# Optimization experiments

Measured on AMD Instinct MI355X. Metric: run time of the kernel, lower is better.

Reference implementation:

```python
import jax, jax.numpy as jnp
import numpy as np

B, C, T, W, H = 32, 80, 2048, 128, 512
FRAMES_PER_WORD = T // W  # 16
K = 5  # conv kernel size (Component approximated as Conv1d(k=5)+ReLU)


def conv1d(x, w, b):
    # x: [B, Cin, T], w: [Cout, Cin, K] -> [B, Cout, T] (SAME padding)
    y = jax.lax.conv_general_dilated(
        x, w, window_strides=(1,), padding='SAME',
        dimension_numbers=('NCH', 'OIH', 'NCH'))
    return y + b[None, :, None]


def setup_inputs() -> dict:
    key = jax.random.key(0)
    k1, k2, k3 = jax.random.split(key, 3)
    features = jax.random.normal(k1, (B, C, T), dtype=jnp.float32)
    # word bounds: contiguous equal-length spans [start, end) covering all T frames
    starts = (jnp.arange(W, dtype=jnp.int64) * FRAMES_PER_WORD)
    ends = starts + FRAMES_PER_WORD
    word_bounds = jnp.broadcast_to(jnp.stack([starts, ends])[None], (B, 2, W))
    word_lengths = jnp.full((B,), W, dtype=jnp.int64)
    enc_w = jax.random.normal(k2, (H, C, K), dtype=jnp.float32) * 0.02
    enc_b = jnp.zeros((H,), dtype=jnp.float32)
    dec_w = jax.random.normal(k3, (1, H, K), dtype=jnp.float32) * 0.02
    dec_b = jnp.zeros((1,), dtype=jnp.float32)
    return {'features': features, 'word_bounds': word_bounds,
            'word_lengths': word_lengths, 'enc_w': enc_w, 'enc_b': enc_b,
            'dec_w': dec_w, 'dec_b': dec_b}


def reference(features, word_bounds, word_lengths, enc_w, enc_b, dec_w, dec_b):
    # Frame encoder: Conv1d + ReLU -> [B, H, T]
    frame_embedding = jax.nn.relu(conv1d(features, enc_w, enc_b))
    t = jnp.arange(T)
    start = word_bounds[:, 0, :]  # [B, W]
    end = word_bounds[:, 1, :]    # [B, W]
    # Ragged per-word mean pooling, fused as a masked matmul (segment mean).
    mask = (t[None, None, :] >= start[..., None]) & (t[None, None, :] < end[..., None])  # [B, W, T]
    valid = jnp.arange(W)[None, :] < word_lengths[:, None]  # [B, W]
    maskf = (mask & valid[..., None]).astype(frame_embedding.dtype)
    counts = jnp.maximum(maskf.sum(-1), 1.0)  # [B, W]
    word_embeddings = jnp.einsum('bct,bwt->bcw', frame_embedding, maskf) / counts[:, None, :]
    # Word decoder: Conv1d over the word axis -> [B, 1, W]
    return conv1d(word_embeddings, dec_w, dec_b)
```

## Files before the change

### kernel.cpp

```cpp
#include <hip/hip_runtime.h>

#define B_ 32
#define C_ 80
#define T_ 2048
#define W_ 128
#define H_ 512
#define K_ 5

#define KTOT 400
#define NKI  13
#define TM   128
#define TN   128
#define SF_STRIDE 80
#define SF_ROWS   136
#define SF_ELEMS  (SF_ROWS * SF_STRIDE)
#define ITER_STRIDE (2 * 4 * 64 * 8)
#define BF_ELEMS  (4 * NKI * ITER_STRIDE)

#define RB_FEAT   1024
#define RB_BFRAG  (RB_FEAT + BF_ELEMS / 256)
#define RB_WORDS  (RB_BFRAG + B_)

#define TILE_S 88

typedef _Float16 half8 __attribute__((ext_vector_type(8)));
typedef float    f4v   __attribute__((ext_vector_type(4)));

typedef const __attribute__((address_space(1))) unsigned int guint;
typedef __attribute__((address_space(3))) unsigned int luint;

__global__ __launch_bounds__(256) void prep_all(
    const float* __restrict__ feat, const float* __restrict__ enc_w,
    const int* __restrict__ bounds, const int* __restrict__ lengths,
    _Float16* __restrict__ featT, _Float16* __restrict__ Bf,
    int* __restrict__ word_of, float* __restrict__ inv_cnt)
{
    __shared__ _Float16 tile[64 * TILE_S];
    const int bid = blockIdx.x;
    const int tid = threadIdx.x;

    if (bid < RB_FEAT) {
        const int b = bid >> 5, tc = bid & 31;
        const int t0 = tc * 64;
        for (int idx = tid; idx < 80 * 64; idx += 256) {
            int cc = idx >> 6, tt = idx & 63;
            float v = feat[((size_t)b * C_ + cc) * T_ + t0 + tt];
            tile[tt * TILE_S + cc] = (_Float16)v;
        }
        __syncthreads();
        for (int idx = tid; idx < 64 * 10; idx += 256) {
            int tt = idx / 10, g = idx % 10;
            *(f4v*)(featT + ((size_t)b * T_ + t0 + tt) * C_ + g * 8) =
                *(const f4v*)(tile + tt * TILE_S + g * 8);
        }
    } else if (bid < RB_BFRAG) {
        int idx = (bid - RB_FEAT) * 256 + tid;
        int e  = idx & 7;
        int l  = (idx >> 3) & 63;
        int j  = (idx >> 9) & 3;
        int w2 = (idx >> 11) & 1;
        int it = (idx >> 12) % NKI;
        int nt = idx / (NKI << 12);
        int h  = nt * 128 + w2 * 64 + j * 16 + (l & 15);
        int kc = it * 32 + (l >> 4) * 8 + e;
        float v = 0.f;
        if (kc < KTOT) v = enc_w[(h * C_ + kc % 80) * K_ + kc / 80];
        Bf[idx] = (_Float16)v;
    } else {
        const int b = bid - RB_BFRAG;
        int* wob = word_of + b * T_;
        for (int t = tid; t < T_; t += 256) wob[t] = -1;
        __syncthreads();
        if (tid < W_) {
            const int len = lengths[b];
            int s = bounds[(b * 2 + 0) * W_ + tid];
            int e = bounds[(b * 2 + 1) * W_ + tid];
            s = max(s, 0); e = min(e, T_);
            bool valid = (tid < len) && (e > s);
            inv_cnt[b * W_ + tid] = valid ? 1.f / (float)(e - s) : 0.f;
            if (valid)
                for (int t = s; t < e; ++t) wob[t] = tid;
        }
    }
}

__global__ __launch_bounds__(256, 3) void gemm_enc(
    const _Float16* __restrict__ featT,
    const _Float16* __restrict__ Bf,
    const float*    __restrict__ enc_b,
    const int*      __restrict__ word_of,
    const float*    __restrict__ inv_cnt,
    float*          __restrict__ wemb)
{
    __shared__ __attribute__((aligned(16))) _Float16 sf[SF_ELEMS];

    const int tid = threadIdx.x;
    const int bid = blockIdx.x;
    const int xcd = bid & 7;
    const int u   = bid >> 3;
    const int nt  = u & 3;
    const int g   = xcd + ((u >> 2) << 3);
    const int b   = g >> 4;
    const int mt  = g & 15;
    const int t0 = mt * TM;
    const int h0 = nt * TN;

    const int lane = tid & 63;
    const int wid  = tid >> 6;
    const int wm = (wid >> 1) * 64;
    const int wn = (wid & 1) * 64;
    const int w2 = wid & 1;
    const int ml = lane & 15;
    const int q  = lane >> 4;

    {
        const _Float16* fb = featT + (size_t)b * T_ * C_;
        const int fbase = (t0 - 2) * C_;
        const int gmax  = T_ * C_ - 8;
        for (int ch = wid; ch < 22; ch += 4) {
            int loff = (ch << 9) + lane * 8;
            if (loff < SF_ELEMS) {
                int goff = fbase + loff;
                goff = min(max(goff, 0), gmax);
                __builtin_amdgcn_global_load_lds((guint*)(fb + goff),
                                                 (luint*)(sf + (ch << 9)), 16, 0, 0);
            }
        }
    }

    const int bT = b * T_;
    const int bW = b * W_;
    int wlo[4], whi[4];
    unsigned ownm = 0;
    {
        int wpv[4], wnx[4];
        #pragma unroll
        for (int i = 0; i < 4; ++i) {
            const int tg = t0 + wm + i * 16;
            wlo[i] = word_of[bT + tg];
            whi[i] = word_of[bT + tg + 15];
            wpv[i] = (tg == 0)       ? -2 : word_of[bT + tg - 1];
            wnx[i] = (tg + 16 >= T_) ? -2 : word_of[bT + tg + 16];
        }
        #pragma unroll
        for (int i = 0; i < 4; ++i)
            if (wpv[i] != wlo[i] && wnx[i] != wlo[i]) ownm |= (1u << i);
    }

    const half8* bfp = (const half8*)(Bf + (((nt * NKI) * 2 + w2) * 4 * 64 + lane) * 8);
    half8 bcur[4], bnxt[4];
    #pragma unroll
    for (int j = 0; j < 4; ++j) bcur[j] = bfp[j * 64];
    #pragma unroll
    for (int j = 0; j < 4; ++j) bnxt[j] = bfp[512 + j * 64];

    __syncthreads();

    if (mt == 0) {
        if (tid < 20) ((f4v*)sf)[tid] = (f4v){};
        __syncthreads();
    }
    if (mt == 15) {
        if (tid < 60) ((f4v*)(sf + 130 * SF_STRIDE))[tid] = (f4v){};
        __syncthreads();
    }

    f4v acc[4][4] = {};

    const int abase = (wm + ml) * SF_STRIDE + q * 8;

    half8 acur[4];
    #pragma unroll
    for (int i = 0; i < 4; ++i)
        acur[i] = *(const half8*)(sf + abase + i * 16 * SF_STRIDE);

    #pragma unroll
    for (int it = 0; it < NKI; ++it) {
        half8 anxt[4], bnn[4];
        #pragma unroll
        for (int i = 0; i < 4; ++i)
            anxt[i] = *(const half8*)(sf + abase + (it + 1) * 32 + i * 16 * SF_STRIDE);
        {
            const half8* bn = bfp + (it + 2) * 512;
            #pragma unroll
            for (int j = 0; j < 4; ++j) bnn[j] = bn[j * 64];
        }
        #pragma unroll
        for (int i = 0; i < 4; ++i)
            #pragma unroll
            for (int j = 0; j < 4; ++j)
                acc[i][j] = __builtin_amdgcn_mfma_f32_16x16x32_f16(acur[i], bcur[j], acc[i][j], 0, 0, 0);
        #pragma unroll
        for (int i = 0; i < 4; ++i) acur[i] = anxt[i];
        #pragma unroll
        for (int j = 0; j < 4; ++j) { bcur[j] = bnxt[j]; bnxt[j] = bnn[j]; }
    }

    float bias[4], invp[4];
    #pragma unroll
    for (int j = 0; j < 4; ++j) bias[j] = enc_b[h0 + wn + j * 16 + ml];
    #pragma unroll
    for (int i = 0; i < 4; ++i) invp[i] = inv_cnt[bW + max(wlo[i], 0)];

    #pragma unroll
    for (int i = 0; i < 4; ++i) {
        const int tg = t0 + wm + i * 16;
        const int w0  = wlo[i];
        const int w15 = whi[i];
        if (w0 == w15) {
            if (w0 >= 0) {
                const float inv = invp[i];
                const bool own = (ownm >> i) & 1;
                #pragma unroll
                for (int j = 0; j < 4; ++j) {
                    float s = 0.f;
                    #pragma unroll
                    for (int r = 0; r < 4; ++r) s += fmaxf(acc[i][j][r] + bias[j], 0.f);
                    s += __shfl_down(s, 32, 64);
                    s += __shfl_down(s, 16, 64);
                    if (q == 0) {
                        float val = s * inv;
                        float* dst = &wemb[(size_t)(bW + w0) * H_ + h0 + wn + j * 16 + ml];
                        if (own) *dst = val;
                        else atomicAdd(dst, val);
                    }
                }
            }
        } else {
            #pragma unroll
            for (int j = 0; j < 4; ++j) {
                #pragma unroll
                for (int r = 0; r < 4; ++r) {
                    int t = tg + q * 4 + r;
                    int w = word_of[bT + t];
                    if (w >= 0)
                        atomicAdd(&wemb[(size_t)(bW + w) * H_ + h0 + wn + j * 16 + ml],
                                  fmaxf(acc[i][j][r] + bias[j], 0.f) * inv_cnt[bW + w]);
                }
            }
        }
    }
}

__global__ __launch_bounds__(256) void dec_all(const float* __restrict__ wemb,
                                               const float* __restrict__ dec_w,
                                               const float* __restrict__ dec_b,
                                               float* __restrict__ out) {
    __shared__ float sdw[H_ * K_];
    __shared__ float se[16][8];
    const int bid = blockIdx.x;
    const int b = bid >> 4, ch = bid & 15;
    const int w0 = ch * 8;
    for (int idx = threadIdx.x; idx < H_ * K_; idx += 256) sdw[idx] = dec_w[idx];
    __syncthreads();
    const int wid = threadIdx.x >> 6, lane = threadIdx.x & 63;
    for (int row = wid; row < 12; row += 4) {
        int wq = w0 - 2 + row;
        float a[K_] = {};
        if (wq >= 0 && wq < W_) {
            const float* src = wemb + ((size_t)b * W_ + wq) * H_;
            #pragma unroll
            for (int r = 0; r < H_ / 64; ++r) {
                int h = r * 64 + lane;
                float v = src[h];
                #pragma unroll
                for (int k = 0; k < K_; ++k) a[k] += v * sdw[h * K_ + k];
            }
        }
        #pragma unroll
        for (int k = 0; k < K_; ++k) {
            #pragma unroll
            for (int off = 32; off > 0; off >>= 1) a[k] += __shfl_down(a[k], off, 64);
        }
        if (lane == 0) {
            #pragma unroll
            for (int k = 0; k < K_; ++k) se[row][k] = a[k];
        }
    }
    __syncthreads();
    if (threadIdx.x < 8) {
        int wl = threadIdx.x;
        float acc = dec_b[0];
        #pragma unroll
        for (int k = 0; k < K_; ++k) acc += se[wl + k][k];
        out[b * W_ + w0 + wl] = acc;
    }
}

extern "C" void kernel_launch(void* const* d_in, const int* in_sizes, int n_in,
                              void* d_out, int out_size, void* d_ws, size_t ws_size,
                              hipStream_t stream) {
    const float* feat    = (const float*)d_in[0];
    const int*   bounds  = (const int*)  d_in[1];
    const int*   lengths = (const int*)  d_in[2];
    const float* enc_w   = (const float*)d_in[3];
    const float* enc_b   = (const float*)d_in[4];
    const float* dec_w   = (const float*)d_in[5];
    const float* dec_b   = (const float*)d_in[6];
    float* out = (float*)d_out;

    char* p = (char*)d_ws;
    _Float16* featT = (_Float16*)p;  p += (size_t)B_ * T_ * C_ * 2;
    _Float16* Bf    = (_Float16*)p;  p += (size_t)(BF_ELEMS + 2 * ITER_STRIDE) * 2;
    int* word_of    = (int*)p;       p += (size_t)B_ * T_ * 4;
    float* inv_cnt  = (float*)p;     p += (size_t)B_ * W_ * 4;
    float* wemb     = (float*)p;

    prep_all<<<RB_WORDS, 256, 0, stream>>>(feat, enc_w, bounds, lengths,
                                           featT, Bf, word_of, inv_cnt);
    gemm_enc<<<B_ * (T_ / TM) * (H_ / TN), 256, 0, stream>>>(
        featT, Bf, enc_b, word_of, inv_cnt, wemb);
    dec_all<<<B_ * 16, 256, 0, stream>>>(wemb, dec_w, dec_b, out);
}
```

Measured before the change: 117.9 us.

## Loop over all H tiles per block to reuse staged feature tile

Each block now handles one (batch, time-tile) pair and loops over all four H tiles internally, reusing the shared-memory feature tile and word metadata instead of reloading them in four separate blocks. The grid shrinks to 512 blocks, and the occupancy hint is lowered to two blocks per CU to leave room for the extra bias registers. The block-to-XCD mapping is changed so each XCD handles four batches. The cost is fewer blocks to fill the GPU and a longer serial loop per block, which may reduce parallelism and latency hiding.

```diff
diff --git a/kernel.cpp b/kernel.cpp
--- a/kernel.cpp
+++ b/kernel.cpp
@@ -84,7 +84,7 @@
     }
 }
 
-__global__ __launch_bounds__(256, 3) void gemm_enc(
+__global__ __launch_bounds__(256, 2) void gemm_enc(
     const _Float16* __restrict__ featT,
     const _Float16* __restrict__ Bf,
     const float*    __restrict__ enc_b,
@@ -98,12 +98,9 @@
     const int bid = blockIdx.x;
     const int xcd = bid & 7;
     const int u   = bid >> 3;
-    const int nt  = u & 3;
-    const int g   = xcd + ((u >> 2) << 3);
-    const int b   = g >> 4;
-    const int mt  = g & 15;
+    const int b   = xcd * 4 + (u & 3);
+    const int mt  = u >> 2;
     const int t0 = mt * TM;
-    const int h0 = nt * TN;
 
     const int lane = tid & 63;
     const int wid  = tid >> 6;
@@ -146,13 +143,23 @@
         for (int i = 0; i < 4; ++i)
             if (wpv[i] != wlo[i] && wnx[i] != wlo[i]) ownm |= (1u << i);
     }
-
-    const half8* bfp = (const half8*)(Bf + (((nt * NKI) * 2 + w2) * 4 * 64 + lane) * 8);
+    float invp[4];
+    #pragma unroll
+    for (int i = 0; i < 4; ++i) invp[i] = inv_cnt[bW + max(wlo[i], 0)];
+
+    float biasAll[4][4];
+    #pragma unroll
+    for (int n = 0; n < 4; ++n)
+        #pragma unroll
+        for (int j = 0; j < 4; ++j)
+            biasAll[n][j] = enc_b[n * TN + wn + j * 16 + ml];
+
+    const half8* bfpB = (const half8*)(Bf + ((w2 * 4) * 64 + lane) * 8);
     half8 bcur[4], bnxt[4];
     #pragma unroll
-    for (int j = 0; j < 4; ++j) bcur[j] = bfp[j * 64];
+    for (int j = 0; j < 4; ++j) bcur[j] = bfpB[j * 64];
     #pragma unroll
-    for (int j = 0; j < 4; ++j) bnxt[j] = bfp[512 + j * 64];
+    for (int j = 0; j < 4; ++j) bnxt[j] = bfpB[512 + j * 64];
 
     __syncthreads();
 
@@ -165,77 +172,74 @@
         __syncthreads();
     }
 
-    f4v acc[4][4] = {};
-
     const int abase = (wm + ml) * SF_STRIDE + q * 8;
 
-    half8 acur[4];
-    #pragma unroll
-    for (int i = 0; i < 4; ++i)
-        acur[i] = *(const half8*)(sf + abase + i * 16 * SF_STRIDE);
-
-    #pragma unroll
-    for (int it = 0; it < NKI; ++it) {
-        half8 anxt[4], bnn[4];
+    for (int nt4 = 0; nt4 < 4; ++nt4) {
+        f4v acc[4][4] = {};
+
+        half8 acur[4];
         #pragma unroll
         for (int i = 0; i < 4; ++i)
-            anxt[i] = *(const half8*)(sf + abase + (it + 1) * 32 + i * 16 * SF_STRIDE);
-        {
-            const half8* bn = bfp + (it + 2) * 512;
-            #pragma unroll
-            for (int j = 0; j < 4; ++j) bnn[j] = bn[j * 64];
-        }
-        #pragma unroll
-        for (int i = 0; i < 4; ++i)
-            #pragma unroll
-            for (int j = 0; j < 4; ++j)
-                acc[i][j] = __builtin_amdgcn_mfma_f32_16x16x32_f16(acur[i], bcur[j], acc[i][j], 0, 0, 0);
-        #pragma unroll
-        for (int i = 0; i < 4; ++i) acur[i] = anxt[i];
-        #pragma unroll
-        for (int j = 0; j < 4; ++j) { bcur[j] = bnxt[j]; bnxt[j] = bnn[j]; }
-    }
-
-    float bias[4], invp[4];
-    #pragma unroll
-    for (int j = 0; j < 4; ++j) bias[j] = enc_b[h0 + wn + j * 16 + ml];
-    #pragma unroll
-    for (int i = 0; i < 4; ++i) invp[i] = inv_cnt[bW + max(wlo[i], 0)];
-
-    #pragma unroll
-    for (int i = 0; i < 4; ++i) {
-        const int tg = t0 + wm + i * 16;
-        const int w0  = wlo[i];
-        const int w15 = whi[i];
-        if (w0 == w15) {
-            if (w0 >= 0) {
-                const float inv = invp[i];
-                const bool own = (ownm >> i) & 1;
+            acur[i] = *(const half8*)(sf + abase + i * 16 * SF_STRIDE);
+
+        #pragma unroll
+        for (int it = 0; it < NKI; ++it) {
+            half8 anxt[4], bnn[4];
+            #pragma unroll
+            for (int i = 0; i < 4; ++i)
+                anxt[i] = *(const half8*)(sf + abase + (it + 1) * 32 + i * 16 * SF_STRIDE);
+            {
+                const half8* bn = bfpB + (nt4 * NKI + it + 2) * 512;
+                #pragma unroll
+                for (int j = 0; j < 4; ++j) bnn[j] = bn[j * 64];
+            }
+            #pragma unroll
+            for (int i = 0; i < 4; ++i)
+                #pragma unroll
+                for (int j = 0; j < 4; ++j)
+                    acc[i][j] = __builtin_amdgcn_mfma_f32_16x16x32_f16(acur[i], bcur[j], acc[i][j], 0, 0, 0);
+            #pragma unroll
+            for (int i = 0; i < 4; ++i) acur[i] = anxt[i];
+            #pragma unroll
+            for (int j = 0; j < 4; ++j) { bcur[j] = bnxt[j]; bnxt[j] = bnn[j]; }
+        }
+
+        const int h0 = nt4 * TN;
+        #pragma unroll
+        for (int i = 0; i < 4; ++i) {
+            const int tg = t0 + wm + i * 16;
+            const int w0  = wlo[i];
+            const int w15 = whi[i];
+            if (w0 == w15) {
+                if (w0 >= 0) {
+                    const float inv = invp[i];
+                    const bool own = (ownm >> i) & 1;
+                    #pragma unroll
+                    for (int j = 0; j < 4; ++j) {
+                        float s = 0.f;
+                        #pragma unroll
+                        for (int r = 0; r < 4; ++r) s += fmaxf(acc[i][j][r] + biasAll[nt4][j], 0.f);
+                        s += __shfl_down(s, 32, 64);
+                        s += __shfl_down(s, 16, 64);
+                        if (q == 0) {
+                            float val = s * inv;
+                            float* dst = &wemb[(size_t)(bW + w0) * H_ + h0 + wn + j * 16 + ml];
+                            if (own) *dst = val;
+                            else atomicAdd(dst, val);
+                        }
+                    }
+                }
+            } else {
                 #pragma unroll
                 for (int j = 0; j < 4; ++j) {
-                    float s = 0.f;
                     #pragma unroll
-                    for (int r = 0; r < 4; ++r) s += fmaxf(acc[i][j][r] + bias[j], 0.f);
-                    s += __shfl_down(s, 32, 64);
-                    s += __shfl_down(s, 16, 64);
-                    if (q == 0) {
-                        float val = s * inv;
-                        float* dst = &wemb[(size_t)(bW + w0) * H_ + h0 + wn + j * 16 + ml];
-                        if (own) *dst = val;
-                        else atomicAdd(dst, val);
+                    for (int r = 0; r < 4; ++r) {
+                        int t = tg + q * 4 + r;
+                        int w = word_of[bT + t];
+                        if (w >= 0)
+                            atomicAdd(&wemb[(size_t)(bW + w) * H_ + h0 + wn + j * 16 + ml],
+                                      fmaxf(acc[i][j][r] + biasAll[nt4][j], 0.f) * inv_cnt[bW + w]);
                     }
-                }
-            }
-        } else {
-            #pragma unroll
-            for (int j = 0; j < 4; ++j) {
-                #pragma unroll
-                for (int r = 0; r < 4; ++r) {
-                    int t = tg + q * 4 + r;
-                    int w = word_of[bT + t];
-                    if (w >= 0)
-                        atomicAdd(&wemb[(size_t)(bW + w) * H_ + h0 + wn + j * 16 + ml],
-                                  fmaxf(acc[i][j][r] + bias[j], 0.f) * inv_cnt[bW + w]);
                 }
             }
         }
@@ -308,7 +312,7 @@
 
     prep_all<<<RB_WORDS, 256, 0, stream>>>(feat, enc_w, bounds, lengths,
                                            featT, Bf, word_of, inv_cnt);
-    gemm_enc<<<B_ * (T_ / TM) * (H_ / TN), 256, 0, stream>>>(
+    gemm_enc<<<B_ * (T_ / TM), 256, 0, stream>>>(
         featT, Bf, enc_b, word_of, inv_cnt, wemb);
     dec_all<<<B_ * 16, 256, 0, stream>>>(wemb, dec_w, dec_b, out);
 }
```

Measured after the change: 167.4 us. 1.42x slower.

## Load GEMM A-fragments directly from global memory instead of staging in LDS

Applied to the files above, without the earlier changes.

Removes the shared-memory staging of the feature tile (global_load_lds plus barriers and edge zeroing). Each lane now reads its A fragments straight from global memory, with clamping and zero-masking at the sequence edges. This drops the LDS footprint and the block syncs, which may allow higher occupancy. The cost is more global/L2 traffic from overlapping reads, and global-load latency inside the MFMA loop that was previously hidden by LDS.

```diff
diff --git a/kernel.cpp b/kernel.cpp
--- a/kernel.cpp
+++ b/kernel.cpp
@@ -11,9 +11,6 @@
 #define NKI  13
 #define TM   128
 #define TN   128
-#define SF_STRIDE 80
-#define SF_ROWS   136
-#define SF_ELEMS  (SF_ROWS * SF_STRIDE)
 #define ITER_STRIDE (2 * 4 * 64 * 8)
 #define BF_ELEMS  (4 * NKI * ITER_STRIDE)
 
@@ -25,9 +22,6 @@
 
 typedef _Float16 half8 __attribute__((ext_vector_type(8)));
 typedef float    f4v   __attribute__((ext_vector_type(4)));
-
-typedef const __attribute__((address_space(1))) unsigned int guint;
-typedef __attribute__((address_space(3))) unsigned int luint;
 
 __global__ __launch_bounds__(256) void prep_all(
     const float* __restrict__ feat, const float* __restrict__ enc_w,
@@ -92,8 +86,6 @@
     const float*    __restrict__ inv_cnt,
     float*          __restrict__ wemb)
 {
-    __shared__ __attribute__((aligned(16))) _Float16 sf[SF_ELEMS];
-
     const int tid = threadIdx.x;
     const int bid = blockIdx.x;
     const int xcd = bid & 7;
@@ -113,20 +105,19 @@
     const int ml = lane & 15;
     const int q  = lane >> 4;
 
-    {
-        const _Float16* fb = featT + (size_t)b * T_ * C_;
-        const int fbase = (t0 - 2) * C_;
-        const int gmax  = T_ * C_ - 8;
-        for (int ch = wid; ch < 22; ch += 4) {
-            int loff = (ch << 9) + lane * 8;
-            if (loff < SF_ELEMS) {
-                int goff = fbase + loff;
-                goff = min(max(goff, 0), gmax);
-                __builtin_amdgcn_global_load_lds((guint*)(fb + goff),
-                                                 (luint*)(sf + (ch << 9)), 16, 0, 0);
-            }
-        }
-    }
+    const half8* bfp = (const half8*)(Bf + (((nt * NKI) * 2 + w2) * 4 * 64 + lane) * 8);
+    half8 bcur[4], bnxt[4];
+    #pragma unroll
+    for (int j = 0; j < 4; ++j) bcur[j] = bfp[j * 64];
+    #pragma unroll
+    for (int j = 0; j < 4; ++j) bnxt[j] = bfp[512 + j * 64];
+
+    const _Float16* fb0 = featT + (size_t)b * T_ * C_;
+    const int rtb   = t0 + wm + ml;
+    const int gbase = (rtb - 2) * C_ + q * 8;
+    const bool edge_lo = (mt == 0  && wm == 0);
+    const bool edge_hi = (mt == 15 && wm == 64);
+    const int gmax = T_ * C_ - 8;
 
     const int bT = b * T_;
     const int bW = b * W_;
@@ -147,39 +138,35 @@
             if (wpv[i] != wlo[i] && wnx[i] != wlo[i]) ownm |= (1u << i);
     }
 
-    const half8* bfp = (const half8*)(Bf + (((nt * NKI) * 2 + w2) * 4 * 64 + lane) * 8);
-    half8 bcur[4], bnxt[4];
-    #pragma unroll
-    for (int j = 0; j < 4; ++j) bcur[j] = bfp[j * 64];
-    #pragma unroll
-    for (int j = 0; j < 4; ++j) bnxt[j] = bfp[512 + j * 64];
-
-    __syncthreads();
-
-    if (mt == 0) {
-        if (tid < 20) ((f4v*)sf)[tid] = (f4v){};
-        __syncthreads();
-    }
-    if (mt == 15) {
-        if (tid < 60) ((f4v*)(sf + 130 * SF_STRIDE))[tid] = (f4v){};
-        __syncthreads();
-    }
-
     f4v acc[4][4] = {};
 
-    const int abase = (wm + ml) * SF_STRIDE + q * 8;
+#define LOAD_A(dst, itv)                                                      \
+    {                                                                         \
+        _Pragma("unroll")                                                     \
+        for (int i = 0; i < 4; ++i) {                                         \
+            int ga = gbase + i * (16 * C_) + (itv) * 32;                      \
+            if ((i == 0 && edge_lo) || (i == 3 && edge_hi)) {                 \
+                int gac = min(max(ga, 0), gmax);                              \
+                half8 v = *(const half8*)(fb0 + gac);                         \
+                int dt = ((itv) * 32 + q * 8) / 80 - 2;                       \
+                int tsrc = rtb + i * 16 + dt;                                 \
+                if ((unsigned)tsrc >= (unsigned)T_) v = (half8){};            \
+                dst[i] = v;                                                   \
+            } else {                                                          \
+                dst[i] = *(const half8*)(fb0 + ga);                           \
+            }                                                                 \
+        }                                                                     \
+    }
 
     half8 acur[4];
-    #pragma unroll
-    for (int i = 0; i < 4; ++i)
-        acur[i] = *(const half8*)(sf + abase + i * 16 * SF_STRIDE);
+    LOAD_A(acur, 0)
 
     #pragma unroll
     for (int it = 0; it < NKI; ++it) {
         half8 anxt[4], bnn[4];
-        #pragma unroll
-        for (int i = 0; i < 4; ++i)
-            anxt[i] = *(const half8*)(sf + abase + (it + 1) * 32 + i * 16 * SF_STRIDE);
+        if (it < NKI - 1) {
+            LOAD_A(anxt, it + 1)
+        }
         {
             const half8* bn = bfp + (it + 2) * 512;
             #pragma unroll
@@ -190,11 +177,14 @@
             #pragma unroll
             for (int j = 0; j < 4; ++j)
                 acc[i][j] = __builtin_amdgcn_mfma_f32_16x16x32_f16(acur[i], bcur[j], acc[i][j], 0, 0, 0);
-        #pragma unroll
-        for (int i = 0; i < 4; ++i) acur[i] = anxt[i];
+        if (it < NKI - 1) {
+            #pragma unroll
+            for (int i = 0; i < 4; ++i) acur[i] = anxt[i];
+        }
         #pragma unroll
         for (int j = 0; j < 4; ++j) { bcur[j] = bnxt[j]; bnxt[j] = bnn[j]; }
     }
+#undef LOAD_A
 
     float bias[4], invp[4];
     #pragma unroll
```

After: 173.2 us. +46.9%, slower.
